# Optimization experiments

Measured on AMD Instinct MI355X. Metric: run time of the kernel, lower is better.

The kernel has to match this reference:

```python
import jax, jax.numpy as jnp
import numpy as np

V, E, H, R, RD = 32000, 300, 300, 50, 50  # vocab, word-emb, hidden, rel vocab, rel emb
B, N = 32, 128                            # trees per batch, nodes per tree


def setup_inputs() -> dict:
    key = jax.random.key(0)
    ks = jax.random.split(key, 10)
    root_hidden = jax.random.normal(ks[0], (B, H), jnp.float32)
    relations = jax.random.randint(ks[1], (B, N), 0, R, jnp.int32)
    prev_words = jax.random.randint(ks[2], (B, N), 0, V, jnp.int32)
    # topologically sorted parent pointers: parent[i] in [-1, i-1]; -1 = virtual root
    rng = np.random.default_rng(0)
    parents = np.full((B, N), -1, dtype=np.int32)
    for i in range(1, N):
        parents[:, i] = rng.integers(-1, i, size=B)
    parents = jnp.asarray(parents)
    s_in = 1.0 / np.float32(np.sqrt(RD + E))
    s_h = 1.0 / np.float32(np.sqrt(H))
    emb = jax.random.normal(ks[3], (V, E), jnp.float32) * 0.02
    rel_emb = jax.random.normal(ks[4], (R, RD), jnp.float32) * 0.02
    W_ih = jax.random.normal(ks[5], (4 * H, RD + E), jnp.float32) * s_in
    W_hh = jax.random.normal(ks[6], (4 * H, H), jnp.float32) * s_h
    b_ih = jnp.zeros((4 * H,), jnp.float32)
    b_hh = jnp.zeros((4 * H,), jnp.float32)
    W_out = jax.random.normal(ks[7], (V, H), jnp.float32) * s_h
    b_out = jnp.zeros((V,), jnp.float32)
    return {"root_hidden": root_hidden, "relations": relations, "prev_words": prev_words,
            "parents": parents, "emb": emb, "rel_emb": rel_emb, "W_ih": W_ih, "W_hh": W_hh,
            "b_ih": b_ih, "b_hh": b_hh, "W_out": W_out, "b_out": b_out}


def reference(root_hidden, relations, prev_words, parents, emb, rel_emb,
              W_ih, W_hh, b_ih, b_hh, W_out, b_out):
    # per-node input: rel embedding ++ (teacher-forced) previous word embedding
    x = jnp.concatenate([rel_emb[relations], emb[prev_words]], axis=-1)  # [B,N,RD+E]
    xg = jnp.einsum('bni,gi->bng', x, W_ih) + b_ih                       # [B,N,4H]

    def one_tree(h0, xg_t, pars):
        n = pars.shape[0]
        h_buf = jnp.zeros((n + 1, H), xg_t.dtype).at[0].set(h0)
        c_buf = jnp.zeros((n + 1, H), xg_t.dtype).at[0].set(h0)  # original: hidden=(h,h)

        def step(carry, inp):
            hb, cb = carry
            xg_i, par, idx = inp
            ph = hb[par + 1]
            pc = cb[par + 1]
            gates = xg_i + ph @ W_hh.T + b_hh
            i_g, f_g, g_g, o_g = jnp.split(gates, 4)
            c = jax.nn.sigmoid(f_g) * pc + jax.nn.sigmoid(i_g) * jnp.tanh(g_g)
            h = jax.nn.sigmoid(o_g) * jnp.tanh(c)
            return (hb.at[idx + 1].set(h), cb.at[idx + 1].set(c)), h

        _, hs = jax.lax.scan(step, (h_buf, c_buf), (xg_t, pars, jnp.arange(n)))
        return hs  # [N,H]

    hs = jax.vmap(one_tree)(root_hidden, xg, parents)          # [B,N,H]
    logits = jnp.einsum('bnh,vh->bnv', hs, W_out) + b_out      # [B,N,V]
    return logits
```

## Files before the change

kernel.cpp:

```cpp
#include <hip/hip_runtime.h>
#include <hip/hip_bf16.h>

typedef unsigned short u16;
typedef unsigned int u32;
typedef unsigned long long u64;
typedef __attribute__((ext_vector_type(8))) short short8;
typedef __attribute__((ext_vector_type(4))) float f32x4;

#define NB 32
#define NN 128
#define HH 300
#define NV 32000
#define KP 320
#define KX 352
#define XGS 1280

#define NSLICE 15
#define UPS 20
#define NROWS 80
#define TPBS 320
#define GMAXN 16
#define LDW 328

#define A_LD(p)     __hip_atomic_load((p), __ATOMIC_RELAXED, __HIP_MEMORY_SCOPE_AGENT)
#define A_ST(p, v)  __hip_atomic_store((p), (v), __ATOMIC_RELAXED, __HIP_MEMORY_SCOPE_AGENT)
#define A_ADD(p, v) __hip_atomic_fetch_add((p), (v), __ATOMIC_RELAXED, __HIP_MEMORY_SCOPE_AGENT)

__device__ __forceinline__ float sigm(float x) { return 1.f / (1.f + __expf(-x)); }
__device__ __forceinline__ float tanh_f(float x) {
    float e = __expf(2.f * x);
    return 1.f - 2.f / (e + 1.f);
}
__device__ __forceinline__ u16 f2bf(float f) {
    __hip_bfloat16 b = __float2bfloat16(f);
    return *reinterpret_cast<u16*>(&b);
}
__device__ __forceinline__ void gl_lds16(const u16* gsrc, u16* ldst) {
    __builtin_amdgcn_global_load_lds(
        (const __attribute__((address_space(1))) void*)gsrc,
        (__attribute__((address_space(3))) void*)ldst, 16, 0, 0);
}

__global__ __launch_bounds__(256) void k_prelude(const float* __restrict__ rh,
                                                 const int* __restrict__ relations,
                                                 const int* __restrict__ prev_words,
                                                 const float* __restrict__ rel_emb,
                                                 const float* __restrict__ emb,
                                                 const float* __restrict__ W_ih,
                                                 const float* __restrict__ W_hh,
                                                 const float* __restrict__ W_out,
                                                 u16* __restrict__ hb16,
                                                 int* __restrict__ lvl_done,
                                                 u16* __restrict__ Wihp,
                                                 u16* __restrict__ Wp16,
                                                 u16* __restrict__ Xbf,
                                                 u16* __restrict__ Bbf) {
    const int stride = gridDim.x * blockDim.x;
    const int idx = blockIdx.x * blockDim.x + threadIdx.x;
    for (int e = idx; e < NB * 129 * 20; e += stride) {
        int row = e / 20, c = 300 + (e - row * 20);
        hb16[(size_t)row * KP + c] = 0;
    }
    for (int e = idx; e < NB * HH; e += stride) {
        int b = e / HH, u = e - b * HH;
        hb16[(size_t)(b * 129) * KP + u] = f2bf(rh[e]);
    }
    for (int e = idx; e < NB * NN; e += stride) lvl_done[e] = 0;
    for (int n = idx; n < 1280 * KX; n += stride) {
        int r = n / KX, k = n - r * KX;
        float v = (r < 1200 && k < 350) ? W_ih[r * 350 + k] : 0.f;
        Wihp[n] = f2bf(v);
    }
    for (int m = idx; m < NSLICE * NROWS * LDW; m += stride) {
        int s = m / (NROWS * LDW);
        int rem = m - s * (NROWS * LDW);
        int r = rem / LDW, k = rem - r * LDW;
        int g = r / UPS, ul = r - g * UPS;
        int grow = g * HH + s * UPS + ul;
        float v = (k < HH) ? W_hh[grow * HH + k] : 0.f;
        Wp16[m] = f2bf(v);
    }
    for (int e = idx; e < NB * NN * KX; e += stride) {
        int node = e / KX, c = e - node * KX;
        float v = 0.f;
        if (c < 50) v = rel_emb[relations[node] * 50 + c];
        else if (c < 350) v = emb[(size_t)prev_words[node] * 300 + (c - 50)];
        Xbf[e] = f2bf(v);
    }
    u64* Bq = (u64*)Bbf;
    for (int e = idx; e < NV * KP / 4; e += stride) {
        const int c4 = e * 4;
        const int v = c4 / KP, k = c4 - v * KP;
        const float* wr = W_out + (size_t)v * HH;
        float x0 = (k + 0 < HH) ? wr[k + 0] : 0.f;
        float x1 = (k + 1 < HH) ? wr[k + 1] : 0.f;
        float x2 = (k + 2 < HH) ? wr[k + 2] : 0.f;
        float x3 = (k + 3 < HH) ? wr[k + 3] : 0.f;
        Bq[e] = (u64)f2bf(x0) | ((u64)f2bf(x1) << 16) |
                ((u64)f2bf(x2) << 32) | ((u64)f2bf(x3) << 48);
    }
}

__global__ void k_prep(const int* __restrict__ parents, int* __restrict__ lvl_nodes,
                       int* __restrict__ lvl_cnt, int* __restrict__ lvl_start,
                       int* __restrict__ nlev) {
    __shared__ int dep[NB][NN];
    __shared__ int cnt[NB][NN];
    __shared__ int st[NB][NN];
    const int t = threadIdx.x;
    if (t < NB) {
        for (int l = 0; l < NN; ++l) cnt[t][l] = 0;
        int md = 0;
        for (int i = 0; i < NN; ++i) {
            int p = parents[t * NN + i];
            int d = (p < 0) ? 0 : dep[t][p] + 1;
            dep[t][i] = d;
            cnt[t][d]++;
            md = max(md, d);
        }
        nlev[t] = md + 1;
        int run = 0;
        for (int l = 0; l < NN; ++l) {
            st[t][l] = run;
            lvl_start[t * NN + l] = run;
            lvl_cnt[t * NN + l] = cnt[t][l];
            run += cnt[t][l];
        }
        for (int i = 0; i < NN; ++i) {
            int d = dep[t][i];
            lvl_nodes[t * NN + st[t][d]] = i;
            st[t][d]++;
        }
    }
}

__global__ __launch_bounds__(256) void k_xgemm(const u16* __restrict__ Xbf,
                                               const u16* __restrict__ Wihp,
                                               const float* __restrict__ b_ih,
                                               float* __restrict__ xg) {
    __shared__ __align__(16) u16 As[128 * 40];
    __shared__ __align__(16) u16 Bs[128 * 40];
    const int tid = threadIdx.x;
    const int lane = tid & 63, wv = tid >> 6;
    const int wm = wv >> 1, wn = wv & 1;
    const int mblk = blockIdx.x, nblk = blockIdx.y;
    const u16* Ag = Xbf + (size_t)mblk * 128 * KX;
    const u16* Bg = Wihp + (size_t)nblk * 128 * KX;
    f32x4 acc[4][4] = {};
    const int lrow = lane & 15, lseg = lane >> 4;
    for (int kk = 0; kk < KX; kk += 32) {
#pragma unroll
        for (int q = 0; q < 2; ++q) {
            int s = tid + q * 256;
            int r = s >> 2, seg = s & 3;
            *(uint4*)&As[r * 40 + seg * 8] = *(const uint4*)&Ag[(size_t)r * KX + kk + seg * 8];
            *(uint4*)&Bs[r * 40 + seg * 8] = *(const uint4*)&Bg[(size_t)r * KX + kk + seg * 8];
        }
        __syncthreads();
        short8 av[4], bv[4];
#pragma unroll
        for (int i = 0; i < 4; ++i) {
            av[i] = *(const short8*)&As[(wm * 64 + i * 16 + lrow) * 40 + lseg * 8];
            bv[i] = *(const short8*)&Bs[(wn * 64 + i * 16 + lrow) * 40 + lseg * 8];
        }
#pragma unroll
        for (int i = 0; i < 4; ++i)
#pragma unroll
            for (int j = 0; j < 4; ++j)
                acc[i][j] = __builtin_amdgcn_mfma_f32_16x16x32_bf16(bv[j], av[i], acc[i][j],
                                                                    0, 0, 0);
        __syncthreads();
    }
#pragma unroll
    for (int i = 0; i < 4; ++i) {
        const int row = mblk * 128 + wm * 64 + i * 16 + lrow;
        float* orow = xg + (size_t)row * XGS;
#pragma unroll
        for (int j = 0; j < 4; ++j) {
            const int col = nblk * 128 + wn * 64 + j * 16 + lseg * 4;
            f32x4 v = acc[i][j];
            if (col < 1200) {
                f32x4 bo = *(const f32x4*)&b_ih[col];
                v[0] += bo[0]; v[1] += bo[1]; v[2] += bo[2]; v[3] += bo[3];
            }
            *(f32x4*)&orow[col] = v;
        }
    }
}

__global__ __launch_bounds__(TPBS) void k_scan(const int* __restrict__ parents,
                                               const u16* __restrict__ Wp16,
                                               const float* __restrict__ xg,
                                               const float* __restrict__ b_hh,
                                               const float* __restrict__ rh,
                                               u16* __restrict__ hb16,
                                               const int* __restrict__ lvl_nodes,
                                               const int* __restrict__ lvl_cnt,
                                               const int* __restrict__ lvl_start,
                                               const int* __restrict__ nlev,
                                               int* __restrict__ lvl_done) {
    __shared__ __align__(16) u16 Wl[NROWS * LDW];
    __shared__ __align__(16) u16 hs[GMAXN * LDW];
    __shared__ __align__(16) float gates[GMAXN * 82];
    __shared__ float c_lds[129 * UPS];
    __shared__ int nid_s[GMAXN], par_s[GMAXN];

    const int t = threadIdx.x;
    const int b = blockIdx.x / NSLICE;
    const int s = blockIdx.x % NSLICE;
    const int lane = t & 63, wv = t >> 6;
    const int lrow = lane & 15, lk = lane >> 4;

    {
        const u64* src = (const u64*)(Wp16 + (size_t)s * NROWS * LDW);
        u64* dst = (u64*)Wl;
        for (int e = t; e < NROWS * LDW / 4; e += TPBS) dst[e] = src[e];
    }
    if (t < UPS) c_lds[t] = rh[b * HH + s * UPS + t];
    __syncthreads();

    const int nl = nlev[b];
    for (int l = 0; l < nl; ++l) {
        const int cnt = lvl_cnt[b * NN + l];
        const int start = lvl_start[b * NN + l];
        for (int off = 0; off < cnt; off += GMAXN) {
            const int gc = min(GMAXN, cnt - off);
            if (t < gc) {
                int i = lvl_nodes[b * NN + start + off + t];
                nid_s[t] = i;
                par_s[t] = parents[b * NN + i];
            }
            __syncthreads();
            for (int e = t; e < gc * 80; e += TPBS) {
                const int j = e / 80, q = e - j * 80;
                const u64* hrow = (const u64*)(hb16 +
                    (size_t)(b * 129 + par_s[j] + 1) * KP);
                *(u64*)&hs[j * LDW + q * 4] = A_LD(&hrow[q]);
            }
            __syncthreads();
            {
                f32x4 acc = {};
#pragma unroll
                for (int kk = 0; kk < KP; kk += 32) {
                    short8 av = *(const short8*)&hs[lrow * LDW + kk + lk * 8];
                    short8 bv = *(const short8*)&Wl[(wv * 16 + lrow) * LDW + kk + lk * 8];
                    acc = __builtin_amdgcn_mfma_f32_16x16x32_bf16(av, bv, acc, 0, 0, 0);
                }
#pragma unroll
                for (int r = 0; r < 4; ++r)
                    gates[(lk * 4 + r) * 82 + wv * 16 + lrow] = acc[r];
            }
            __syncthreads();
            if (t < 160) {
                const int j = t / 10, up = t - j * 10;
                if (j < gc) {
                    const int i = nid_s[j];
                    const int par = par_s[j];
                    const int ul0 = up * 2;
                    const float* gj = gates + j * 82;
                    const float* xgp = xg + (size_t)(b * NN + i) * XGS + s * UPS;
                    const float* bhp = b_hh + s * UPS;
                    float hv[2];
#pragma unroll
                    for (int un = 0; un < 2; ++un) {
                        const int ul = ul0 + un;
                        float gs[4];
#pragma unroll
                        for (int g = 0; g < 4; ++g)
                            gs[g] = gj[g * UPS + ul] + xgp[g * HH + ul] + bhp[g * HH + ul];
                        const float pc = c_lds[(par + 1) * UPS + ul];
                        const float cv = sigm(gs[1]) * pc + sigm(gs[0]) * tanh_f(gs[2]);
                        hv[un] = sigm(gs[3]) * tanh_f(cv);
                        c_lds[(i + 1) * UPS + ul] = cv;
                    }
                    const u32 hp = (u32)f2bf(hv[0]) | ((u32)f2bf(hv[1]) << 16);
                    A_ST((u32*)(hb16 + (size_t)(b * 129 + i + 1) * KP + s * UPS + ul0), hp);
                }
            }
            __syncthreads();
        }
        if (l + 1 < nl) {
            if (t == 0) {
                int* dp = &lvl_done[b * NN + l];
                const int old = A_ADD(dp, 1);
                if (old != NSLICE - 1) {
                    while (A_LD(dp) < NSLICE) __builtin_amdgcn_s_sleep(1);
                }
            }
            __syncthreads();
        }
    }
}

__global__ __launch_bounds__(256) void k_gemm(const u16* __restrict__ hb16,
                                              const u16* __restrict__ Bbf,
                                              const float* __restrict__ b_out,
                                              float* __restrict__ out) {
    __shared__ __align__(16) u16 As[128 * 32];
    __shared__ __align__(16) u16 Bs[128 * 32];
    const int tid = threadIdx.x;
    const int lane = tid & 63, wv = tid >> 6;
    const int wm = wv >> 1, wn = wv & 1;
    const int bid = blockIdx.x;
    const int newbid = (bid & 7) * 1000 + (bid >> 3);
    const int mblk = newbid & 31, nblk = newbid >> 5;
    const u16* Ag = hb16 + ((size_t)mblk * 129 + 1) * KP;
    const u16* Bg = Bbf + (size_t)nblk * 128 * KP;
    const int r0 = wv * 32 + (lane >> 2);
    const int r1 = r0 + 16;
    const int q0 = lane & 3;
    const int lk0 = (q0 - (r0 >> 1)) & 3;
    const int lk1 = (q0 - (r1 >> 1)) & 3;
    const u16* pa0 = Ag + (size_t)r0 * KP + lk0 * 8;
    const u16* pa1 = Ag + (size_t)r1 * KP + lk1 * 8;
    const u16* pb0 = Bg + (size_t)r0 * KP + lk0 * 8;
    const u16* pb1 = Bg + (size_t)r1 * KP + lk1 * 8;
    u16* lA = As + wv * 1024;
    u16* lB = Bs + wv * 1024;
    f32x4 acc[4][4] = {};
    const int lrow = lane & 15, lseg = lane >> 4;
    for (int kk = 0; kk < KP; kk += 32) {
        gl_lds16(pa0 + kk, lA);
        gl_lds16(pa1 + kk, lA + 512);
        gl_lds16(pb0 + kk, lB);
        gl_lds16(pb1 + kk, lB + 512);
        __syncthreads();
        short8 av[4], bv[4];
#pragma unroll
        for (int i = 0; i < 4; ++i) {
            const int ra = wm * 64 + i * 16 + lrow;
            const int rb = wn * 64 + i * 16 + lrow;
            av[i] = *(const short8*)&As[ra * 32 + (((lseg + (ra >> 1)) & 3) * 8)];
            bv[i] = *(const short8*)&Bs[rb * 32 + (((lseg + (rb >> 1)) & 3) * 8)];
        }
#pragma unroll
        for (int i = 0; i < 4; ++i)
#pragma unroll
            for (int j = 0; j < 4; ++j)
                acc[i][j] = __builtin_amdgcn_mfma_f32_16x16x32_bf16(bv[j], av[i], acc[i][j],
                                                                    0, 0, 0);
        __syncthreads();
    }
#pragma unroll
    for (int i = 0; i < 4; ++i) {
        const int row = mblk * 128 + wm * 64 + i * 16 + lrow;
        float* orow = out + (size_t)row * NV;
#pragma unroll
        for (int j = 0; j < 4; ++j) {
            const int col = nblk * 128 + wn * 64 + j * 16 + lseg * 4;
            f32x4 v = acc[i][j];
            f32x4 bo = *(const f32x4*)&b_out[col];
            v[0] += bo[0]; v[1] += bo[1]; v[2] += bo[2]; v[3] += bo[3];
            __builtin_nontemporal_store(v, (f32x4*)&orow[col]);
        }
    }
}

extern "C" void kernel_launch(void* const* d_in, const int* in_sizes, int n_in,
                              void* d_out, int out_size, void* d_ws, size_t ws_size,
                              hipStream_t stream) {
    const float* root_hidden = (const float*)d_in[0];
    const int* relations = (const int*)d_in[1];
    const int* prev_words = (const int*)d_in[2];
    const int* parents = (const int*)d_in[3];
    const float* emb = (const float*)d_in[4];
    const float* rel_emb = (const float*)d_in[5];
    const float* W_ih = (const float*)d_in[6];
    const float* W_hh = (const float*)d_in[7];
    const float* b_ih = (const float*)d_in[8];
    const float* b_hh = (const float*)d_in[9];
    const float* W_out = (const float*)d_in[10];
    const float* b_out = (const float*)d_in[11];
    float* out = (float*)d_out;

    float* xg = (float*)d_ws;
    u16* Xbf = (u16*)(xg + 4096 * XGS);
    u16* Wihp = Xbf + 4096 * KX;
    u16* Wp16 = Wihp + 1280 * KX;
    u16* hb16 = Wp16 + NSLICE * NROWS * LDW;
    u16* Bbf = hb16 + 1320960;
    int* lvl_nodes = (int*)(Bbf + 10240000);
    int* lvl_cnt = lvl_nodes + 4096;
    int* lvl_start = lvl_cnt + 4096;
    int* nlev = lvl_start + 4096;
    int* lvl_done = nlev + 64;

    k_prelude<<<2048, 256, 0, stream>>>(root_hidden, relations, prev_words, rel_emb, emb,
                                        W_ih, W_hh, W_out, hb16, lvl_done, Wihp, Wp16,
                                        Xbf, Bbf);
    k_prep<<<1, 64, 0, stream>>>(parents, lvl_nodes, lvl_cnt, lvl_start, nlev);

    k_xgemm<<<dim3(32, 10), 256, 0, stream>>>(Xbf, Wihp, b_ih, xg);

    k_scan<<<dim3(NB * NSLICE), dim3(TPBS), 0, stream>>>(
        parents, Wp16, xg, b_hh, root_hidden, hb16,
        lvl_nodes, lvl_cnt, lvl_start, nlev, lvl_done);

    k_gemm<<<dim3(8000), 256, 0, stream>>>(hb16, Bbf, b_out, out);
}
```

Measured before the change: 328.4 us.

## Prefetch early-ready parent states before level barrier and fuse prep kernels

Moves the tree level analysis into the prelude kernel. It also moves the W_out bf16 cast into extra blocks of the xgemm kernel, which removes a launch and lets the cast overlap the GEMM. In the scan, nodes of each level are sorted so that those whose parent sits at an earlier level (already final) come first. Their parent hidden rows are gathered into LDS before waiting on the cross-block level barrier, which shortens the critical path per level. The cost is extra bookkeeping (lvl_split), more per-thread private arrays in the single-block prelude analysis, and a more complex staging path.

```diff
diff --git a/kernel.cpp b/kernel.cpp
--- a/kernel.cpp
+++ b/kernel.cpp
@@ -48,13 +48,17 @@
                                                  const float* __restrict__ emb,
                                                  const float* __restrict__ W_ih,
                                                  const float* __restrict__ W_hh,
-                                                 const float* __restrict__ W_out,
+                                                 const int* __restrict__ parents,
                                                  u16* __restrict__ hb16,
                                                  int* __restrict__ lvl_done,
                                                  u16* __restrict__ Wihp,
                                                  u16* __restrict__ Wp16,
                                                  u16* __restrict__ Xbf,
-                                                 u16* __restrict__ Bbf) {
+                                                 int* __restrict__ lvl_nodes,
+                                                 int* __restrict__ lvl_cnt,
+                                                 int* __restrict__ lvl_start,
+                                                 int* __restrict__ lvl_split,
+                                                 int* __restrict__ nlev) {
     const int stride = gridDim.x * blockDim.x;
     const int idx = blockIdx.x * blockDim.x + threadIdx.x;
     for (int e = idx; e < NB * 129 * 20; e += stride) {
@@ -87,63 +91,68 @@
         else if (c < 350) v = emb[(size_t)prev_words[node] * 300 + (c - 50)];
         Xbf[e] = f2bf(v);
     }
-    u64* Bq = (u64*)Bbf;
-    for (int e = idx; e < NV * KP / 4; e += stride) {
-        const int c4 = e * 4;
-        const int v = c4 / KP, k = c4 - v * KP;
-        const float* wr = W_out + (size_t)v * HH;
-        float x0 = (k + 0 < HH) ? wr[k + 0] : 0.f;
-        float x1 = (k + 1 < HH) ? wr[k + 1] : 0.f;
-        float x2 = (k + 2 < HH) ? wr[k + 2] : 0.f;
-        float x3 = (k + 3 < HH) ? wr[k + 3] : 0.f;
-        Bq[e] = (u64)f2bf(x0) | ((u64)f2bf(x1) << 16) |
-                ((u64)f2bf(x2) << 32) | ((u64)f2bf(x3) << 48);
-    }
-}
-
-__global__ void k_prep(const int* __restrict__ parents, int* __restrict__ lvl_nodes,
-                       int* __restrict__ lvl_cnt, int* __restrict__ lvl_start,
-                       int* __restrict__ nlev) {
-    __shared__ int dep[NB][NN];
-    __shared__ int cnt[NB][NN];
-    __shared__ int st[NB][NN];
-    const int t = threadIdx.x;
-    if (t < NB) {
-        for (int l = 0; l < NN; ++l) cnt[t][l] = 0;
+    if (blockIdx.x == 0 && threadIdx.x < NB) {
+        const int tb = threadIdx.x;
+        const int* par = parents + tb * NN;
+        int dep[NN], cnt[NN], st[NN], ec[NN], ce[NN], cl[NN];
+        for (int l = 0; l < NN; ++l) { cnt[l] = 0; ec[l] = 0; }
         int md = 0;
         for (int i = 0; i < NN; ++i) {
-            int p = parents[t * NN + i];
-            int d = (p < 0) ? 0 : dep[t][p] + 1;
-            dep[t][i] = d;
-            cnt[t][d]++;
+            int p = par[i];
+            int d = (p < 0) ? 0 : dep[p] + 1;
+            dep[i] = d;
+            cnt[d]++;
+            if (p < 0 || dep[p] < d - 1) ec[d]++;
             md = max(md, d);
         }
-        nlev[t] = md + 1;
+        nlev[tb] = md + 1;
         int run = 0;
         for (int l = 0; l < NN; ++l) {
-            st[t][l] = run;
-            lvl_start[t * NN + l] = run;
-            lvl_cnt[t * NN + l] = cnt[t][l];
-            run += cnt[t][l];
+            st[l] = run;
+            lvl_start[tb * NN + l] = run;
+            lvl_cnt[tb * NN + l] = cnt[l];
+            lvl_split[tb * NN + l] = ec[l];
+            ce[l] = run;
+            cl[l] = run + ec[l];
+            run += cnt[l];
         }
         for (int i = 0; i < NN; ++i) {
-            int d = dep[t][i];
-            lvl_nodes[t * NN + st[t][d]] = i;
-            st[t][d]++;
-        }
-    }
-}
-
-__global__ __launch_bounds__(256) void k_xgemm(const u16* __restrict__ Xbf,
-                                               const u16* __restrict__ Wihp,
-                                               const float* __restrict__ b_ih,
-                                               float* __restrict__ xg) {
+            int d = dep[i], p = par[i];
+            bool early = (p < 0) || (dep[p] < d - 1);
+            lvl_nodes[tb * NN + (early ? ce[d]++ : cl[d]++)] = i;
+        }
+    }
+}
+
+__global__ __launch_bounds__(256) void k_xgemm_cast(const u16* __restrict__ Xbf,
+                                                    const u16* __restrict__ Wihp,
+                                                    const float* __restrict__ b_ih,
+                                                    float* __restrict__ xg,
+                                                    const float* __restrict__ W_out,
+                                                    u16* __restrict__ Bbf) {
     __shared__ __align__(16) u16 As[128 * 40];
     __shared__ __align__(16) u16 Bs[128 * 40];
     const int tid = threadIdx.x;
+    if (blockIdx.x >= 320) {
+        const int cidx = (blockIdx.x - 320) * 256 + tid;
+        const int cstride = 512 * 256;
+        u64* Bq = (u64*)Bbf;
+        for (int e = cidx; e < NV * KP / 4; e += cstride) {
+            const int c4 = e * 4;
+            const int v = c4 / KP, k = c4 - v * KP;
+            const float* wr = W_out + (size_t)v * HH;
+            float x0 = (k + 0 < HH) ? wr[k + 0] : 0.f;
+            float x1 = (k + 1 < HH) ? wr[k + 1] : 0.f;
+            float x2 = (k + 2 < HH) ? wr[k + 2] : 0.f;
+            float x3 = (k + 3 < HH) ? wr[k + 3] : 0.f;
+            Bq[e] = (u64)f2bf(x0) | ((u64)f2bf(x1) << 16) |
+                    ((u64)f2bf(x2) << 32) | ((u64)f2bf(x3) << 48);
+        }
+        return;
+    }
     const int lane = tid & 63, wv = tid >> 6;
     const int wm = wv >> 1, wn = wv & 1;
-    const int mblk = blockIdx.x, nblk = blockIdx.y;
+    const int mblk = blockIdx.x % 32, nblk = blockIdx.x / 32;
     const u16* Ag = Xbf + (size_t)mblk * 128 * KX;
     const u16* Bg = Wihp + (size_t)nblk * 128 * KX;
     f32x4 acc[4][4] = {};
@@ -197,6 +206,7 @@
                                                const int* __restrict__ lvl_nodes,
                                                const int* __restrict__ lvl_cnt,
                                                const int* __restrict__ lvl_start,
+                                               const int* __restrict__ lvl_split,
                                                const int* __restrict__ nlev,
                                                int* __restrict__ lvl_done) {
     __shared__ __align__(16) u16 Wl[NROWS * LDW];
@@ -210,6 +220,7 @@
     const int s = blockIdx.x % NSLICE;
     const int lane = t & 63, wv = t >> 6;
     const int lrow = lane & 15, lk = lane >> 4;
+    const int base = b * NN;
 
     {
         const u64* src = (const u64*)(Wp16 + (size_t)s * NROWS * LDW);
@@ -217,25 +228,50 @@
         for (int e = t; e < NROWS * LDW / 4; e += TPBS) dst[e] = src[e];
     }
     if (t < UPS) c_lds[t] = rh[b * HH + s * UPS + t];
-    __syncthreads();
+
+    {
+        const int gc0 = min(GMAXN, lvl_cnt[base]);
+        if (t < gc0) {
+            int i = lvl_nodes[base + t];
+            nid_s[t] = i;
+            par_s[t] = parents[base + i];
+        }
+        __syncthreads();
+        for (int e = t; e < gc0 * 80; e += TPBS) {
+            const int j = e / 80, q = e - j * 80;
+            const u64* hrow = (const u64*)(hb16 + (size_t)(b * 129 + par_s[j] + 1) * KP);
+            *(u64*)&hs[j * LDW + q * 4] = A_LD(&hrow[q]);
+        }
+    }
 
     const int nl = nlev[b];
     for (int l = 0; l < nl; ++l) {
-        const int cnt = lvl_cnt[b * NN + l];
-        const int start = lvl_start[b * NN + l];
+        const int cnt = lvl_cnt[base + l];
+        const int start = lvl_start[base + l];
+        const int split = lvl_split[base + l];
         for (int off = 0; off < cnt; off += GMAXN) {
             const int gc = min(GMAXN, cnt - off);
-            if (t < gc) {
-                int i = lvl_nodes[b * NN + start + off + t];
-                nid_s[t] = i;
-                par_s[t] = parents[b * NN + i];
-            }
-            __syncthreads();
-            for (int e = t; e < gc * 80; e += TPBS) {
-                const int j = e / 80, q = e - j * 80;
-                const u64* hrow = (const u64*)(hb16 +
-                    (size_t)(b * 129 + par_s[j] + 1) * KP);
-                *(u64*)&hs[j * LDW + q * 4] = A_LD(&hrow[q]);
+            if (off == 0) {
+                const int es = min(split, gc);
+                for (int e = t; e < (gc - es) * 80; e += TPBS) {
+                    const int j = es + e / 80, q = e % 80;
+                    const u64* hrow = (const u64*)(hb16 +
+                        (size_t)(b * 129 + par_s[j] + 1) * KP);
+                    *(u64*)&hs[j * LDW + q * 4] = A_LD(&hrow[q]);
+                }
+            } else {
+                if (t < gc) {
+                    int i = lvl_nodes[base + start + off + t];
+                    nid_s[t] = i;
+                    par_s[t] = parents[base + i];
+                }
+                __syncthreads();
+                for (int e = t; e < gc * 80; e += TPBS) {
+                    const int j = e / 80, q = e - j * 80;
+                    const u64* hrow = (const u64*)(hb16 +
+                        (size_t)(b * 129 + par_s[j] + 1) * KP);
+                    *(u64*)&hs[j * LDW + q * 4] = A_LD(&hrow[q]);
+                }
             }
             __syncthreads();
             {
@@ -258,7 +294,7 @@
                     const int par = par_s[j];
                     const int ul0 = up * 2;
                     const float* gj = gates + j * 82;
-                    const float* xgp = xg + (size_t)(b * NN + i) * XGS + s * UPS;
+                    const float* xgp = xg + (size_t)(base + i) * XGS + s * UPS;
                     const float* bhp = b_hh + s * UPS;
                     float hv[2];
 #pragma unroll
@@ -280,8 +316,24 @@
             __syncthreads();
         }
         if (l + 1 < nl) {
+            const int cntN = lvl_cnt[base + l + 1];
+            const int startN = lvl_start[base + l + 1];
+            const int gcN = min(GMAXN, cntN);
+            const int esN = min(lvl_split[base + l + 1], gcN);
+            if (t < gcN) {
+                int i = lvl_nodes[base + startN + t];
+                nid_s[t] = i;
+                par_s[t] = parents[base + i];
+            }
+            __syncthreads();
+            for (int e = t; e < esN * 80; e += TPBS) {
+                const int j = e / 80, q = e - j * 80;
+                const u64* hrow = (const u64*)(hb16 +
+                    (size_t)(b * 129 + par_s[j] + 1) * KP);
+                *(u64*)&hs[j * LDW + q * 4] = A_LD(&hrow[q]);
+            }
             if (t == 0) {
-                int* dp = &lvl_done[b * NN + l];
+                int* dp = &lvl_done[base + l];
                 const int old = A_ADD(dp, 1);
                 if (old != NSLICE - 1) {
                     while (A_LD(dp) < NSLICE) __builtin_amdgcn_s_sleep(1);
@@ -382,19 +434,19 @@
     int* lvl_nodes = (int*)(Bbf + 10240000);
     int* lvl_cnt = lvl_nodes + 4096;
     int* lvl_start = lvl_cnt + 4096;
-    int* nlev = lvl_start + 4096;
+    int* lvl_split = lvl_start + 4096;
+    int* nlev = lvl_split + 4096;
     int* lvl_done = nlev + 64;
 
     k_prelude<<<2048, 256, 0, stream>>>(root_hidden, relations, prev_words, rel_emb, emb,
-                                        W_ih, W_hh, W_out, hb16, lvl_done, Wihp, Wp16,
-                                        Xbf, Bbf);
-    k_prep<<<1, 64, 0, stream>>>(parents, lvl_nodes, lvl_cnt, lvl_start, nlev);
-
-    k_xgemm<<<dim3(32, 10), 256, 0, stream>>>(Xbf, Wihp, b_ih, xg);
+                                        W_ih, W_hh, parents, hb16, lvl_done, Wihp, Wp16,
+                                        Xbf, lvl_nodes, lvl_cnt, lvl_start, lvl_split, nlev);
+
+    k_xgemm_cast<<<832, 256, 0, stream>>>(Xbf, Wihp, b_ih, xg, W_out, Bbf);
 
     k_scan<<<dim3(NB * NSLICE), dim3(TPBS), 0, stream>>>(
         parents, Wp16, xg, b_hh, root_hidden, hb16,
-        lvl_nodes, lvl_cnt, lvl_start, nlev, lvl_done);
+        lvl_nodes, lvl_cnt, lvl_start, lvl_split, nlev, lvl_done);
 
     k_gemm<<<dim3(8000), 256, 0, stream>>>(hb16, Bbf, b_out, out);
 }
```

After: 429.3 us. +30.7%, slower.
